# Kernel optimization log

Hardware: AMD Instinct MI355X
Metric: run time of the kernel (lower is better)

The kernel has to match this reference:

```python
import jax, jax.numpy as jnp
import numpy as np

B, T, D = 64, 2048, 512
H = 64           # hidden_size
K, S = 3, 3      # kernel_size, stride
PAD = (K - 1) // 2
BATCH_FACTOR = 0.5


def _ceil_div(a, b):
    return -(-a // b)


def _conv1d(x, w, b, stride, padding):
    # x: [B, C_in, T], w: [C_out, C_in, K] (torch Conv1d layout), b: [C_out]
    y = jax.lax.conv_general_dilated(
        x, w, window_strides=(stride,), padding=[(padding, padding)],
        dimension_numbers=("NCH", "OIH", "NCH"))
    return y + b[None, :, None]


def _score_estimator(x, seq_lens, w1, b1, w2, b2):
    # x: [B, T, D] -> scores [B, T''], seq lens [B]
    xc = jnp.transpose(x, (0, 2, 1))                     # [B, D, T]
    h = _conv1d(xc, w1, b1, S, PAD)                      # [B, 2H, T']
    h = h.reshape(h.shape[0], H, 2, h.shape[-1]).max(axis=2)  # maxout pairs -> [B, H, T']
    s = _conv1d(h, w2, b2, S, PAD)[:, 0, :]              # [B, T'']
    sl = _ceil_div(seq_lens - K + 1 + 2 * PAD, S)
    sl = _ceil_div(sl - K + 1 + 2 * PAD, S)
    return s, sl


def setup_inputs() -> dict:
    key = jax.random.key(0)
    ks = jax.random.split(key, 6)
    x = jax.random.normal(ks[0], (B, T, D), dtype=jnp.float32)
    seq_lens = jax.random.randint(ks[1], (B,), T // 2, T + 1)
    w1 = jax.random.normal(ks[2], (2 * H, D, K), dtype=jnp.float32) * (1.0 / np.sqrt(D * K))
    b1 = jax.random.normal(ks[3], (2 * H,), dtype=jnp.float32) * 0.01
    w2 = jax.random.normal(ks[4], (1, H, K), dtype=jnp.float32) * (1.0 / np.sqrt(H * K))
    b2 = jax.random.normal(ks[5], (1,), dtype=jnp.float32) * 0.01
    return {"x": x, "seq_lens": seq_lens, "w1": w1, "b1": b1, "w2": w2, "b2": b2}


def reference(x, seq_lens, w1, b1, w2, b2):
    scores, scores_sl = _score_estimator(x, seq_lens, w1, b1, w2, b2)  # [B, T''], [B]
    # mean over (padded) time, rescaled by T''/seq_len (torch true division -> float)
    est = scores.mean(axis=1) * (scores.shape[1] / scores_sl.astype(jnp.float32))  # [B]
    k = int(scores.shape[0] * BATCH_FACTOR)
    _, idx = jax.lax.top_k(est, k)
    # torch builds a boolean mask + masked_select, which preserves original batch order
    idx = jnp.sort(idx)
    sel_lens = seq_lens[idx]                              # [B']
    x_sel = x[idx]                                        # [B', T, D]
    # torch also truncates time to max(sel_lens); drops only padding frames.
    # Done eagerly here (data-dependent shape, so not inside jit).
    max_time = int(jnp.max(sel_lens))
    x_sel = x_sel[:, :max_time, :]
    return x_sel, sel_lens
```

## Files before the change

kernel.cpp:

```cpp
#include <hip/hip_runtime.h>

#define T_LEN 2048
#define D_DIM 512
#define B_SZ  64
#define T1_LEN 683
#define NSEL  32
#define KTOT  1536
#define BK    64
#define TILE_T1 96
#define NTILES 8
#define NITER (KTOT / BK)

typedef __attribute__((ext_vector_type(8))) short bf16x8;
typedef __attribute__((ext_vector_type(4))) float f32x4;

constexpr size_t OFF_WHI = 0;
constexpr size_t OFF_WLO = 393216;
constexpr size_t OFF_EST = 786432;
constexpr size_t OFF_SEL = 786944;
constexpr size_t OFF_ZERO = 787072;

__device__ inline unsigned bf16_rne(float x) {
    unsigned u = __float_as_uint(x);
    return (u + 0x7FFFu + ((u >> 16) & 1u)) >> 16;
}

__device__ __forceinline__ void gload_lds16(const void* g, void* l) {
    __builtin_amdgcn_global_load_lds(
        (const __attribute__((address_space(1))) unsigned int*)g,
        (__attribute__((address_space(3))) unsigned int*)l,
        16, 0, 0);
}

__global__ __launch_bounds__(256) void pack_w1_split(const float* __restrict__ w1,
                                                     unsigned short* __restrict__ whi,
                                                     unsigned short* __restrict__ wlo,
                                                     float* __restrict__ est_raw,
                                                     float* __restrict__ zbuf) {
    if (blockIdx.x == 0 && threadIdx.x < 64) est_raw[threadIdx.x] = 0.f;
    if (blockIdx.x == 0 && threadIdx.x >= 64 && threadIdx.x < 128) zbuf[threadIdx.x - 64] = 0.f;
    int idx = blockIdx.x * 256 + threadIdx.x;
    int k0blk = idx >> 13;
    int rem   = idx & 8191;
    int row   = rem >> 6;
    int col   = rem & 63;
    int c8s   = col >> 3;
    int e     = col & 7;
    int c8    = c8s ^ (row & 7);
    int kap   = (k0blk << 6) + (c8 << 3) + e;
    int k = kap >> 9, d = kap & 511;
    float v = w1[row * 1536 + d * 3 + k];
    unsigned hb = bf16_rne(v);
    float hf = __uint_as_float(hb << 16);
    whi[idx] = (unsigned short)hb;
    wlo[idx] = (unsigned short)bf16_rne(v - hf);
}

__global__ __launch_bounds__(256, 2) void conv1_mfma(
        const float* __restrict__ x,
        const unsigned short* __restrict__ whi,
        const unsigned short* __restrict__ wlo,
        const float* __restrict__ b1,
        const float* __restrict__ w2,
        float* __restrict__ est_raw,
        const float* __restrict__ zbuf) {
    __shared__ __align__(16) unsigned short Ahi[128 * 64];
    __shared__ __align__(16) unsigned short Alo[128 * 64];
    __shared__ __align__(16) float Bf[96 * 64];
    __shared__ float b1s[128];
    __shared__ float w2s[192];
    __shared__ float red[256];

    const int tid  = threadIdx.x;
    const int lane = tid & 63;
    const int w    = tid >> 6;
    const int b    = blockIdx.y;
    const int t1g0 = blockIdx.x * TILE_T1;

    if (tid < 128) b1s[tid] = b1[tid];
    if (tid < 192) w2s[tid] = w2[tid];

    const float* xb = x + (size_t)b * (T_LEN * (size_t)D_DIM);

    const int l15  = lane & 15;
    const int quad = lane >> 4;
    const int c0w  = (w >> 1) * 64;
    const int t0w  = (w & 1) * 48;

    int offA[4], swA[4];
    #pragma unroll
    for (int mi = 0; mi < 4; ++mi) { int r = c0w + mi * 16 + l15; offA[mi] = r * 64; swA[mi] = r & 7; }
    int rBo[3], jB[3];
    #pragma unroll
    for (int ni = 0; ni < 3; ++ni) { int r = t0w + ni * 16 + l15; rBo[ni] = r * 64; jB[ni] = r & 15; }

    int bbase[6], bthr[6];
    float* bdst[6];
    #pragma unroll
    for (int i = 0; i < 6; ++i) {
        int row   = w * 24 + i * 4 + (lane >> 4);
        int t1abs = t1g0 + row;
        int c     = (lane & 15) ^ (row & 15);
        bbase[i]  = 1536 * t1abs + c * 4 - 512;
        bthr[i]   = (t1abs < T1_LEN) ? (512 - c * 4 - 1536 * t1abs) : 0x7FFFFFFF;
        bdst[i]   = Bf + (w * 1536 + i * 256 + lane * 4);
    }

    f32x4 acc[4][3];
    #pragma unroll
    for (int mi = 0; mi < 4; ++mi)
        #pragma unroll
        for (int ni = 0; ni < 3; ++ni) acc[mi][ni] = (f32x4){0.f, 0.f, 0.f, 0.f};

    for (int it = 0; it < NITER; ++it) {
        const int k0 = it * BK;

        #pragma unroll
        for (int i = 0; i < 6; ++i) {
            const float* s = (k0 >= bthr[i]) ? (xb + (bbase[i] + k0)) : zbuf;
            gload_lds16(s, bdst[i]);
        }
        {
            const unsigned short* sH = whi + it * 8192 + tid * 8;
            const unsigned short* sL = wlo + it * 8192 + tid * 8;
            unsigned short* dH = Ahi + tid * 8;
            unsigned short* dL = Alo + tid * 8;
            #pragma unroll
            for (int s = 0; s < 4; ++s) {
                gload_lds16(sH + s * 2048, dH + s * 2048);
                gload_lds16(sL + s * 2048, dL + s * 2048);
            }
        }
        __syncthreads();

        #pragma unroll
        for (int ks = 0; ks < 2; ++ks) {
            const int ch = ks * 4 + quad;
            bf16x8 ah[4], al[4], bh[3], bl[3];
            #pragma unroll
            for (int mi = 0; mi < 4; ++mi) {
                int o = offA[mi] + ((ch ^ swA[mi]) << 3);
                ah[mi] = *(const bf16x8*)(Ahi + o);
                al[mi] = *(const bf16x8*)(Alo + o);
            }
            #pragma unroll
            for (int ni = 0; ni < 3; ++ni) {
                int p0 = ((2 * ch)     ^ jB[ni]) << 2;
                int p1 = ((2 * ch + 1) ^ jB[ni]) << 2;
                float4 va = *(const float4*)(Bf + rBo[ni] + p0);
                float4 vb = *(const float4*)(Bf + rBo[ni] + p1);
                unsigned f0 = __float_as_uint(va.x), f1 = __float_as_uint(va.y);
                unsigned f2 = __float_as_uint(va.z), f3 = __float_as_uint(va.w);
                unsigned f4 = __float_as_uint(vb.x), f5 = __float_as_uint(vb.y);
                unsigned f6 = __float_as_uint(vb.z), f7 = __float_as_uint(vb.w);
                unsigned hp0 = __builtin_amdgcn_perm(f1, f0, 0x07060302u);
                unsigned hp1 = __builtin_amdgcn_perm(f3, f2, 0x07060302u);
                unsigned hp2 = __builtin_amdgcn_perm(f5, f4, 0x07060302u);
                unsigned hp3 = __builtin_amdgcn_perm(f7, f6, 0x07060302u);
                float r0 = va.x - __uint_as_float(f0 & 0xFFFF0000u);
                float r1 = va.y - __uint_as_float(f1 & 0xFFFF0000u);
                float r2 = va.z - __uint_as_float(f2 & 0xFFFF0000u);
                float r3 = va.w - __uint_as_float(f3 & 0xFFFF0000u);
                float r4 = vb.x - __uint_as_float(f4 & 0xFFFF0000u);
                float r5 = vb.y - __uint_as_float(f5 & 0xFFFF0000u);
                float r6 = vb.z - __uint_as_float(f6 & 0xFFFF0000u);
                float r7 = vb.w - __uint_as_float(f7 & 0xFFFF0000u);
                unsigned lp0 = __builtin_amdgcn_perm(__float_as_uint(r1), __float_as_uint(r0), 0x07060302u);
                unsigned lp1 = __builtin_amdgcn_perm(__float_as_uint(r3), __float_as_uint(r2), 0x07060302u);
                unsigned lp2 = __builtin_amdgcn_perm(__float_as_uint(r5), __float_as_uint(r4), 0x07060302u);
                unsigned lp3 = __builtin_amdgcn_perm(__float_as_uint(r7), __float_as_uint(r6), 0x07060302u);
                int4 hv = make_int4(hp0, hp1, hp2, hp3);
                int4 lv = make_int4(lp0, lp1, lp2, lp3);
                bh[ni] = __builtin_bit_cast(bf16x8, hv);
                bl[ni] = __builtin_bit_cast(bf16x8, lv);
            }
            #pragma unroll
            for (int mi = 0; mi < 4; ++mi)
                #pragma unroll
                for (int ni = 0; ni < 3; ++ni) {
                    acc[mi][ni] = __builtin_amdgcn_mfma_f32_16x16x32_bf16(ah[mi], bh[ni], acc[mi][ni], 0, 0, 0);
                    acc[mi][ni] = __builtin_amdgcn_mfma_f32_16x16x32_bf16(ah[mi], bl[ni], acc[mi][ni], 0, 0, 0);
                    acc[mi][ni] = __builtin_amdgcn_mfma_f32_16x16x32_bf16(al[mi], bh[ni], acc[mi][ni], 0, 0, 0);
                }
        }
        __syncthreads();
    }

    float contrib = 0.f;
    #pragma unroll
    for (int mi = 0; mi < 4; ++mi) {
        const int cbase = c0w + mi * 16 + (quad << 2);
        const float bb0 = b1s[cbase], bb1 = b1s[cbase + 1];
        const float bb2 = b1s[cbase + 2], bb3 = b1s[cbase + 3];
        const int j0 = cbase >> 1;
        #pragma unroll
        for (int ni = 0; ni < 3; ++ni) {
            const int t1 = t1g0 + t0w + ni * 16 + l15;
            if (t1 < T1_LEN) {
                float p0 = fmaxf(acc[mi][ni][0] + bb0, acc[mi][ni][1] + bb1);
                float p1 = fmaxf(acc[mi][ni][2] + bb2, acc[mi][ni][3] + bb3);
                int r = (t1 + 1) % 3;
                contrib += p0 * w2s[j0 * 3 + r] + p1 * w2s[(j0 + 1) * 3 + r];
            }
        }
    }
    red[tid] = contrib;
    __syncthreads();
    for (int off = 128; off > 0; off >>= 1) {
        if (tid < off) red[tid] += red[tid + off];
        __syncthreads();
    }
    if (tid == 0) atomicAdd(est_raw + b, red[0]);
}

__global__ void select_k(const float* __restrict__ est_raw,
                         const float* __restrict__ b2,
                         const int* __restrict__ seq_lens,
                         int* __restrict__ sel,
                         float* __restrict__ out_lens) {
    const int i = threadIdx.x;
    __shared__ float e[64];
    const int L  = seq_lens[i];
    const int sl = ((L + 2) / 3 + 2) / 3;
    const float ei = (est_raw[i] + 228.0f * b2[0]) / (float)sl;
    e[i] = ei;
    __syncthreads();
    int rank = 0;
    for (int j = 0; j < 64; ++j) {
        float ej = e[j];
        rank += (ej > ei) || (ej == ei && j < i);
    }
    const bool selq = rank < NSEL;
    const unsigned long long m = __ballot(selq);
    if (selq) {
        int pos = __popcll(m & ((1ull << i) - 1ull));
        sel[pos] = i;
        out_lens[pos] = (float)L;
    }
}

__global__ __launch_bounds__(256) void gather_rows(const float* __restrict__ x,
                                                   const int* __restrict__ sel,
                                                   float* __restrict__ out,
                                                   int n4row) {
    const int i = blockIdx.y;
    const int v = blockIdx.x * 256 + threadIdx.x;
    if (v < n4row) {
        const int src = sel[i];
        const float4* xs = (const float4*)(x + (size_t)src * T_LEN * D_DIM);
        float4* od = (float4*)(out + (size_t)i * ((size_t)n4row * 4));
        od[v] = xs[v];
    }
}

extern "C" void kernel_launch(void* const* d_in, const int* in_sizes, int n_in,
                              void* d_out, int out_size, void* d_ws, size_t ws_size,
                              hipStream_t stream) {
    const float* x        = (const float*)d_in[0];
    const int*   seq_lens = (const int*)  d_in[1];
    const float* w1       = (const float*)d_in[2];
    const float* b1       = (const float*)d_in[3];
    const float* w2       = (const float*)d_in[4];
    const float* b2       = (const float*)d_in[5];
    float* out = (float*)d_out;

    char* ws = (char*)d_ws;
    unsigned short* whi = (unsigned short*)(ws + OFF_WHI);
    unsigned short* wlo = (unsigned short*)(ws + OFF_WLO);
    float* est_raw = (float*)(ws + OFF_EST);
    int*   sel     = (int*)  (ws + OFF_SEL);
    float* zbuf    = (float*)(ws + OFF_ZERO);

    const int max_time = (out_size - NSEL) / (NSEL * D_DIM);

    pack_w1_split<<<768, 256, 0, stream>>>(w1, whi, wlo, est_raw, zbuf);
    conv1_mfma<<<dim3(NTILES, B_SZ), 256, 0, stream>>>(x, whi, wlo, b1, w2, est_raw, zbuf);
    select_k<<<1, 64, 0, stream>>>(est_raw, b2, seq_lens, sel,
                                   out + (size_t)NSEL * max_time * D_DIM);
    const int n4row = max_time * (D_DIM / 4);
    gather_rows<<<dim3((n4row + 255) / 256, NSEL), 256, 0, stream>>>(x, sel, out, n4row);
}
```

Before: 448.3 us.

## Double-buffer LDS tiles with halved K-step to overlap loads and MFMA

Halves the K tile from 64 to 32 and splits LDS into two ping-pong buffers for the weight hi/lo tiles and the x tile. The next tile's global-to-LDS loads are issued before computing on the current one, so memory latency can overlap with MFMA work. The weight packing swizzle and the B-tile load mapping are reworked for the narrower tile. It doubles the iteration count and adds per-iteration sync overhead. Total LDS use stays about the same, so occupancy should not change.

```diff
diff --git a/kernel.cpp b/kernel.cpp
--- a/kernel.cpp
+++ b/kernel.cpp
@@ -6,7 +6,7 @@
 #define T1_LEN 683
 #define NSEL  32
 #define KTOT  1536
-#define BK    64
+#define BK    32
 #define TILE_T1 96
 #define NTILES 8
 #define NITER (KTOT / BK)
@@ -40,14 +40,14 @@
     if (blockIdx.x == 0 && threadIdx.x < 64) est_raw[threadIdx.x] = 0.f;
     if (blockIdx.x == 0 && threadIdx.x >= 64 && threadIdx.x < 128) zbuf[threadIdx.x - 64] = 0.f;
     int idx = blockIdx.x * 256 + threadIdx.x;
-    int k0blk = idx >> 13;
-    int rem   = idx & 8191;
-    int row   = rem >> 6;
-    int col   = rem & 63;
-    int c8s   = col >> 3;
+    int k0blk = idx >> 12;
+    int rem   = idx & 4095;
+    int row   = rem >> 5;
+    int col   = rem & 31;
+    int c4s   = col >> 3;
     int e     = col & 7;
-    int c8    = c8s ^ (row & 7);
-    int kap   = (k0blk << 6) + (c8 << 3) + e;
+    int c4    = c4s ^ (row & 3);
+    int kap   = (k0blk << 5) + (c4 << 3) + e;
     int k = kap >> 9, d = kap & 511;
     float v = w1[row * 1536 + d * 3 + k];
     unsigned hb = bf16_rne(v);
@@ -64,9 +64,12 @@
         const float* __restrict__ w2,
         float* __restrict__ est_raw,
         const float* __restrict__ zbuf) {
-    __shared__ __align__(16) unsigned short Ahi[128 * 64];
-    __shared__ __align__(16) unsigned short Alo[128 * 64];
-    __shared__ __align__(16) float Bf[96 * 64];
+    __shared__ __align__(16) unsigned short Ahi0[128 * 32];
+    __shared__ __align__(16) unsigned short Ahi1[128 * 32];
+    __shared__ __align__(16) unsigned short Alo0[128 * 32];
+    __shared__ __align__(16) unsigned short Alo1[128 * 32];
+    __shared__ __align__(16) float Bf0[96 * 32];
+    __shared__ __align__(16) float Bf1[96 * 32];
     __shared__ float b1s[128];
     __shared__ float w2s[192];
     __shared__ float red[256];
@@ -89,21 +92,22 @@
 
     int offA[4], swA[4];
     #pragma unroll
-    for (int mi = 0; mi < 4; ++mi) { int r = c0w + mi * 16 + l15; offA[mi] = r * 64; swA[mi] = r & 7; }
+    for (int mi = 0; mi < 4; ++mi) { int r = c0w + mi * 16 + l15; offA[mi] = r * 32; swA[mi] = r & 3; }
     int rBo[3], jB[3];
     #pragma unroll
-    for (int ni = 0; ni < 3; ++ni) { int r = t0w + ni * 16 + l15; rBo[ni] = r * 64; jB[ni] = r & 15; }
-
-    int bbase[6], bthr[6];
-    float* bdst[6];
-    #pragma unroll
-    for (int i = 0; i < 6; ++i) {
-        int row   = w * 24 + i * 4 + (lane >> 4);
+    for (int ni = 0; ni < 3; ++ni) { int r = t0w + ni * 16 + l15; rBo[ni] = r * 32; jB[ni] = r & 7; }
+
+    const int pB   = tid & 7;
+    const int rw7  = (tid >> 3) & 7;
+    const int cB   = pB ^ rw7;
+    int bbase[3], bthr[3], bfo[3];
+    #pragma unroll
+    for (int i = 0; i < 3; ++i) {
+        int row   = (tid >> 3) + 32 * i;
         int t1abs = t1g0 + row;
-        int c     = (lane & 15) ^ (row & 15);
-        bbase[i]  = 1536 * t1abs + c * 4 - 512;
-        bthr[i]   = (t1abs < T1_LEN) ? (512 - c * 4 - 1536 * t1abs) : 0x7FFFFFFF;
-        bdst[i]   = Bf + (w * 1536 + i * 256 + lane * 4);
+        bbase[i]  = 1536 * t1abs + cB * 4 - 512;
+        bthr[i]   = (t1abs < T1_LEN) ? (512 - cB * 4 - 1536 * t1abs) : 0x7FFFFFFF;
+        bfo[i]    = tid * 4 + 1024 * i;
     }
 
     f32x4 acc[4][3];
@@ -112,43 +116,60 @@
         #pragma unroll
         for (int ni = 0; ni < 3; ++ni) acc[mi][ni] = (f32x4){0.f, 0.f, 0.f, 0.f};
 
+    {
+        #pragma unroll
+        for (int i = 0; i < 3; ++i) {
+            const float* s = (0 >= bthr[i]) ? (xb + bbase[i]) : zbuf;
+            gload_lds16(s, Bf0 + bfo[i]);
+        }
+        const unsigned short* sH = whi + tid * 8;
+        const unsigned short* sL = wlo + tid * 8;
+        gload_lds16(sH,        Ahi0 + tid * 8);
+        gload_lds16(sH + 2048, Ahi0 + tid * 8 + 2048);
+        gload_lds16(sL,        Alo0 + tid * 8);
+        gload_lds16(sL + 2048, Alo0 + tid * 8 + 2048);
+    }
+    __syncthreads();
+
+    #pragma unroll 2
     for (int it = 0; it < NITER; ++it) {
-        const int k0 = it * BK;
-
-        #pragma unroll
-        for (int i = 0; i < 6; ++i) {
-            const float* s = (k0 >= bthr[i]) ? (xb + (bbase[i] + k0)) : zbuf;
-            gload_lds16(s, bdst[i]);
+        const int cu = it & 1;
+        const unsigned short* AhiC = cu ? Ahi1 : Ahi0;
+        const unsigned short* AloC = cu ? Alo1 : Alo0;
+        const float*          BfC  = cu ? Bf1  : Bf0;
+
+        if (it + 1 < NITER) {
+            unsigned short* AhiN = cu ? Ahi0 : Ahi1;
+            unsigned short* AloN = cu ? Alo0 : Alo1;
+            float*          BfN  = cu ? Bf0  : Bf1;
+            const int k0n = (it + 1) * BK;
+            #pragma unroll
+            for (int i = 0; i < 3; ++i) {
+                const float* s = (k0n >= bthr[i]) ? (xb + (bbase[i] + k0n)) : zbuf;
+                gload_lds16(s, BfN + bfo[i]);
+            }
+            const unsigned short* sH = whi + (it + 1) * 4096 + tid * 8;
+            const unsigned short* sL = wlo + (it + 1) * 4096 + tid * 8;
+            gload_lds16(sH,        AhiN + tid * 8);
+            gload_lds16(sH + 2048, AhiN + tid * 8 + 2048);
+            gload_lds16(sL,        AloN + tid * 8);
+            gload_lds16(sL + 2048, AloN + tid * 8 + 2048);
         }
+
         {
-            const unsigned short* sH = whi + it * 8192 + tid * 8;
-            const unsigned short* sL = wlo + it * 8192 + tid * 8;
-            unsigned short* dH = Ahi + tid * 8;
-            unsigned short* dL = Alo + tid * 8;
-            #pragma unroll
-            for (int s = 0; s < 4; ++s) {
-                gload_lds16(sH + s * 2048, dH + s * 2048);
-                gload_lds16(sL + s * 2048, dL + s * 2048);
-            }
-        }
-        __syncthreads();
-
-        #pragma unroll
-        for (int ks = 0; ks < 2; ++ks) {
-            const int ch = ks * 4 + quad;
             bf16x8 ah[4], al[4], bh[3], bl[3];
             #pragma unroll
             for (int mi = 0; mi < 4; ++mi) {
-                int o = offA[mi] + ((ch ^ swA[mi]) << 3);
-                ah[mi] = *(const bf16x8*)(Ahi + o);
-                al[mi] = *(const bf16x8*)(Alo + o);
+                int o = offA[mi] + ((quad ^ swA[mi]) << 3);
+                ah[mi] = *(const bf16x8*)(AhiC + o);
+                al[mi] = *(const bf16x8*)(AloC + o);
             }
             #pragma unroll
             for (int ni = 0; ni < 3; ++ni) {
-                int p0 = ((2 * ch)     ^ jB[ni]) << 2;
-                int p1 = ((2 * ch + 1) ^ jB[ni]) << 2;
-                float4 va = *(const float4*)(Bf + rBo[ni] + p0);
-                float4 vb = *(const float4*)(Bf + rBo[ni] + p1);
+                int p0 = ((2 * quad)     ^ jB[ni]) << 2;
+                int p1 = ((2 * quad + 1) ^ jB[ni]) << 2;
+                float4 va = *(const float4*)(BfC + rBo[ni] + p0);
+                float4 vb = *(const float4*)(BfC + rBo[ni] + p1);
                 unsigned f0 = __float_as_uint(va.x), f1 = __float_as_uint(va.y);
                 unsigned f2 = __float_as_uint(va.z), f3 = __float_as_uint(va.w);
                 unsigned f4 = __float_as_uint(vb.x), f5 = __float_as_uint(vb.y);
```

After: 444.3 us. About the same (-0.9%).
